# Performance work log

Measured on AMD Instinct MI355X. Metric: run time of the kernel, lower is better.

The kernel has to match this reference:

```python
import jax, jax.numpy as jnp
import numpy as np

N = 100_000      # n_nodes
DEG = 32         # edge_threshold (fixed out-degree)
D = 64           # in_channels = out_channels, heads = 1
NEG_SLOPE = 0.2


def setup_inputs() -> dict:
    key = jax.random.key(0)
    k1, k2, k3, k4 = jax.random.split(key, 4)
    x = jax.random.normal(k1, (N, D), jnp.float32)
    # fixed-degree edge list with no self loops (offset in [1, N-1])
    src = jnp.repeat(jnp.arange(N, dtype=jnp.int64), DEG)
    off = jax.random.randint(k2, (N * DEG,), 1, N, dtype=jnp.int64)
    dst = (src + off) % N
    edge_index = jnp.stack([src, dst])  # [2, E]
    # glorot init as in the torch module
    stdv_w = float(np.sqrt(6.0 / (D + D)))
    weight = jax.random.uniform(k3, (D, D), jnp.float32, -stdv_w, stdv_w)
    stdv_a = float(np.sqrt(6.0 / (1 + 2 * D)))  # att is [1, heads=1, 2*D]
    att = jax.random.uniform(k4, (2 * D,), jnp.float32, -stdv_a, stdv_a)
    bias = jnp.zeros((D,), jnp.float32)
    return {"x": x, "edge_index": edge_index, "weight": weight, "att": att, "bias": bias}


def reference(x, edge_index, weight, att, bias):
    n, d = x.shape
    h = x @ weight                               # [N, D] (heads=1)
    # add self loops (inputs are constructed without self loops)
    loop = jnp.arange(n, dtype=edge_index.dtype)
    src = jnp.concatenate([edge_index[0], loop])  # message sources (x_j)
    dst = jnp.concatenate([edge_index[1], loop])  # aggregation targets (x_i)
    # GAT edge score: (cat([x_i, x_j]) * att).sum(-1) = h_i@a_i + h_j@a_j
    a_i, a_j = att[:d], att[d:]
    s_i = h @ a_i                                 # [N]
    s_j = h @ a_j                                 # [N]
    alpha = s_i[dst] + s_j[src]                   # [E+N]
    alpha = jnp.where(alpha > 0, alpha, NEG_SLOPE * alpha)  # leaky_relu
    # segment softmax over destination nodes (numerically stable)
    amax = jax.ops.segment_max(alpha, dst, num_segments=n)
    e = jnp.exp(alpha - amax[dst])
    denom = jax.ops.segment_sum(e, dst, num_segments=n)
    w = e / (denom[dst] + 1e-16)                  # [E+N]
    # weighted scatter-add aggregation of source features
    out = jax.ops.segment_sum(h[src] * w[:, None], dst, num_segments=n)  # [N, D]
    out = out + bias                              # head-mean is identity (heads=1)
    # dropout(p=0.5) is identity in eval mode; F.normalize (L2, dim=1, eps=1e-12)
    norm = jnp.linalg.norm(out, axis=1, keepdims=True)
    return out / jnp.maximum(norm, 1e-12)
```

## Files before the change

kernel.cpp:

```cpp
#include <hip/hip_runtime.h>
#include <math.h>

#define NEG_SLOPE 0.2f
#define NBINS_MAX 392
#define CURSOR_PAD 16
#define NCHB 512
#define CHUNK_B 6256
#define CAPL 44
#define STRL 45
#define BIN_CAP 8704
#define CAPN 72
#define STRN 73

__device__ __forceinline__ unsigned pk_bf16x2(float a, float b) {
    unsigned ua = __float_as_uint(a);
    ua = (ua + 0x7FFFu + ((ua >> 16) & 1u)) >> 16;
    unsigned ub = __float_as_uint(b);
    ub = (ub + 0x7FFFu + ((ub >> 16) & 1u)) & 0xFFFF0000u;
    return ua | ub;
}

__global__ __launch_bounds__(512) void k_linbin(
        const float* __restrict__ x, const float* __restrict__ W,
        const float* __restrict__ att,
        uint2* __restrict__ h16, float* __restrict__ si, float* __restrict__ sj,
        const int* __restrict__ src, const int* __restrict__ dst, int E, int nbins,
        int* __restrict__ bin_cursor, unsigned* __restrict__ bin_edges, int n)
{
    __shared__ unsigned bins[NBINS_MAX * STRL];
    __shared__ int cnt[NBINS_MAX];
    __shared__ int gbase[NBINS_MAX];

    int tid = threadIdx.x;

    if (blockIdx.x < NCHB) {
        int base = blockIdx.x * CHUNK_B;
        int cntE = E - base;
        if (cntE > CHUNK_B) cntE = CHUNK_B;
        if (cntE < 0) cntE = 0;
        int c4 = cntE >> 2;

        for (int b = tid; b < nbins; b += 512) cnt[b] = 0;
        __syncthreads();

#define PLACE(dd, ss) { int bb = (dd) >> 8; int c = atomicAdd(&cnt[bb], 1); \
        if (c < CAPL) bins[bb * STRL + c] = ((unsigned)((dd) & 255) << 17) | (unsigned)(ss); }
        {
            const int4* dst4 = (const int4*)(dst + base);
            const int4* src4 = (const int4*)(src + base);
            for (int i = tid; i < c4; i += 512) {
                int4 d4 = dst4[i];
                int4 s4 = src4[i];
                PLACE(d4.x, s4.x) PLACE(d4.y, s4.y) PLACE(d4.z, s4.z) PLACE(d4.w, s4.w)
            }
            for (int i = (c4 << 2) + tid; i < cntE; i += 512) {
                int dd = dst[base + i]; int ss = src[base + i];
                PLACE(dd, ss)
            }
        }
#undef PLACE
        __syncthreads();

        {
            int start = (blockIdx.x * 97) % nbins;
            for (int k = tid; k < nbins; k += 512) {
                int b = k + start;
                if (b >= nbins) b -= nbins;
                int c = cnt[b];
                if (c > CAPL) c = CAPL;
                int g = (c > 0) ? atomicAdd(&bin_cursor[b * CURSOR_PAD], c) : 0;
                int allow = BIN_CAP - g;
                if (allow < 0) allow = 0;
                if (c > allow) c = allow;
                cnt[b] = c;
                gbase[b] = b * BIN_CAP + g;
            }
        }
        __syncthreads();

        int lane = tid & 63;
        int wv = tid >> 6;
        for (int b = wv; b < nbins; b += 8) {
            int c = cnt[b];
            if (lane < c) bin_edges[gbase[b] + lane] = bins[b * STRL + lane];
        }
    } else {
        int lb = blockIdx.x - NCHB;
        int lane = tid & 63;
        int wv = tid >> 6;
        int q = lane >> 4;
        int f = lane & 15;

        const float4* W4 = (const float4*)W;
        float4 Wr[16];
#pragma unroll
        for (int kb = 0; kb < 16; ++kb)
            Wr[kb] = W4[(16 * q + kb) * 16 + f];

        const float4* att4 = (const float4*)att;
        float4 ai4 = att4[f];
        float4 aj4 = att4[16 + f];
        const float4* x4 = (const float4*)x;

        int row0 = (lb * 8 + wv) * 8;
        for (int r = 0; r < 8; ++r) {
            int row = row0 + r;
            if (row >= n) break;
            size_t xb = (size_t)row * 16 + 4 * q;
            float4 xq0 = x4[xb + 0];
            float4 xq1 = x4[xb + 1];
            float4 xq2 = x4[xb + 2];
            float4 xq3 = x4[xb + 3];
            float4 acc = {0.f, 0.f, 0.f, 0.f};
#define LSTEP(xc, kb) { float4 w4 = Wr[kb]; \
        acc.x = fmaf((xc), w4.x, acc.x); acc.y = fmaf((xc), w4.y, acc.y); \
        acc.z = fmaf((xc), w4.z, acc.z); acc.w = fmaf((xc), w4.w, acc.w); }
            LSTEP(xq0.x, 0)  LSTEP(xq0.y, 1)  LSTEP(xq0.z, 2)  LSTEP(xq0.w, 3)
            LSTEP(xq1.x, 4)  LSTEP(xq1.y, 5)  LSTEP(xq1.z, 6)  LSTEP(xq1.w, 7)
            LSTEP(xq2.x, 8)  LSTEP(xq2.y, 9)  LSTEP(xq2.z, 10) LSTEP(xq2.w, 11)
            LSTEP(xq3.x, 12) LSTEP(xq3.y, 13) LSTEP(xq3.z, 14) LSTEP(xq3.w, 15)
#undef LSTEP
            acc.x += __shfl_xor(acc.x, 16); acc.x += __shfl_xor(acc.x, 32);
            acc.y += __shfl_xor(acc.y, 16); acc.y += __shfl_xor(acc.y, 32);
            acc.z += __shfl_xor(acc.z, 16); acc.z += __shfl_xor(acc.z, 32);
            acc.w += __shfl_xor(acc.w, 16); acc.w += __shfl_xor(acc.w, 32);

            if (q == 0) {
                uint2 p;
                p.x = pk_bf16x2(acc.x, acc.y);
                p.y = pk_bf16x2(acc.z, acc.w);
                h16[(size_t)row * 16 + f] = p;
            }

            float p = acc.x * ai4.x + acc.y * ai4.y + acc.z * ai4.z + acc.w * ai4.w;
            float pq = acc.x * aj4.x + acc.y * aj4.y + acc.z * aj4.z + acc.w * aj4.w;
#pragma unroll
            for (int o = 8; o >= 1; o >>= 1) {
                p += __shfl_xor(p, o);
                pq += __shfl_xor(pq, o);
            }
            if (lane == 0) { si[row] = p; sj[row] = pq; }
        }
    }
}

__global__ __launch_bounds__(512) void k_csr(const int* __restrict__ bin_cursor,
        const unsigned* __restrict__ bin_edges, unsigned* __restrict__ cols,
        int* __restrict__ row_start, int* __restrict__ deg, int n)
{
    __shared__ unsigned slots[256 * STRN];
    __shared__ int cntv[256];
    __shared__ int offv[256];
    __shared__ int wsum[4];
    int b = blockIdx.x;
    int tid = threadIdx.x;
    int base = b * BIN_CAP;
    int cntE = bin_cursor[b * CURSOR_PAD];
    if (cntE > BIN_CAP) cntE = BIN_CAP;
    int c4 = cntE >> 2;

    if (tid < 256) cntv[tid] = 0;
    __syncthreads();

#define PUT(pkv) { unsigned pk = (pkv); int nl = (int)(pk >> 17); \
        int c = atomicAdd(&cntv[nl], 1); \
        if (c < CAPN) slots[nl * STRN + c] = pk & 0x1FFFFu; }
    {
        const uint4* be4 = (const uint4*)(bin_edges + base);
        for (int i = tid; i < c4; i += 512) {
            uint4 p = be4[i];
            PUT(p.x) PUT(p.y) PUT(p.z) PUT(p.w)
        }
        for (int i = (c4 << 2) + tid; i < cntE; i += 512)
            PUT(bin_edges[base + i])
    }
#undef PUT
    __syncthreads();

    int lane = tid & 63;
    int wv = tid >> 6;
    int s = 0, v = 0;
    if (tid < 256) {
        s = cntv[tid];
        if (s > CAPN) s = CAPN;
        v = s;
#pragma unroll
        for (int o = 1; o < 64; o <<= 1) {
            int t = __shfl_up(v, o);
            if (lane >= o) v += t;
        }
        if (lane == 63) wsum[wv] = v;
    }
    __syncthreads();
    if (tid < 256) {
        int woff = 0;
        for (int w = 0; w < wv; ++w) woff += wsum[w];
        int ex = v - s + woff;
        int gd = b * 256 + tid;
        if (gd < n) {
            row_start[gd] = base + ex;
            deg[gd] = s;
        }
        offv[tid] = ex;
        cntv[tid] = s;
    }
    __syncthreads();

    for (int nl = wv; nl < 256; nl += 8) {
        int c = cntv[nl];
        int ex = offv[nl];
        if (lane < c)      cols[base + ex + lane]      = slots[nl * STRN + lane];
        if (lane + 64 < c) cols[base + ex + lane + 64] = slots[nl * STRN + lane + 64];
    }
}

__global__ __launch_bounds__(256) void k_agg(const uint2* __restrict__ h16,
        const float* __restrict__ si, const float* __restrict__ sj,
        const int* __restrict__ row_start, const int* __restrict__ deg_arr,
        const unsigned* __restrict__ cols,
        const float* __restrict__ bias, float* __restrict__ out, int n)
{
    __shared__ int2 swArr[4][132];
    int lane = threadIdx.x & 63;
    int wv = threadIdx.x >> 6;
    int d = blockIdx.x * 4 + wv;
    if (d >= n) return;

    int dg = deg_arr[d];
    if (dg > 128) dg = 128;
    int rs = row_start[d];
    float sid = si[d];

    int s0 = 0, s1 = 0;
    float a0 = -1e30f, a1 = -1e30f;
    if (lane < dg) {
        s0 = (int)cols[rs + lane];
        float t = sid + sj[s0];
        a0 = t > 0.f ? t : NEG_SLOPE * t;
    }
    if (lane + 64 < dg) {
        s1 = (int)cols[rs + lane + 64];
        float t = sid + sj[s1];
        a1 = t > 0.f ? t : NEG_SLOPE * t;
    }
    float tself = sid + sj[d];
    float aself = tself > 0.f ? tself : NEG_SLOPE * tself;

    float m = fmaxf(fmaxf(a0, a1), aself);
#pragma unroll
    for (int o = 32; o >= 1; o >>= 1) m = fmaxf(m, __shfl_xor(m, o));

    float e0 = (lane < dg) ? __expf(a0 - m) : 0.f;
    float e1 = (lane + 64 < dg) ? __expf(a1 - m) : 0.f;
    float eself = __expf(aself - m);

    float dsum = e0 + e1;
#pragma unroll
    for (int o = 32; o >= 1; o >>= 1) dsum += __shfl_xor(dsum, o);
    dsum += eself;

    if (lane < dg) swArr[wv][lane] = make_int2(s0, __float_as_int(e0));
    if (lane + 64 < dg) swArr[wv][lane + 64] = make_int2(s1, __float_as_int(e1));
    if (lane == 0) swArr[wv][dg] = make_int2(d, __float_as_int(eself));
    int cntAll = dg + 1;

    int q = lane >> 4;
    int f = lane & 15;
    int fb = f << 3;
    const char* h8 = (const char*)h16;
    float4 acc0 = {0.f, 0.f, 0.f, 0.f};
    float4 acc1 = {0.f, 0.f, 0.f, 0.f};
    float4 acc2 = {0.f, 0.f, 0.f, 0.f};
    float4 acc3 = {0.f, 0.f, 0.f, 0.f};

#define GLOAD(e) (*(const uint2*)(h8 + (((unsigned)(e) << 7) | fb)))
#define UNPK_FMA(hv, wgt, acc) { \
        acc.x = fmaf((wgt), __uint_as_float((hv).x << 16), acc.x); \
        acc.y = fmaf((wgt), __uint_as_float((hv).x & 0xFFFF0000u), acc.y); \
        acc.z = fmaf((wgt), __uint_as_float((hv).y << 16), acc.z); \
        acc.w = fmaf((wgt), __uint_as_float((hv).y & 0xFFFF0000u), acc.w); }

    int j = q;
    for (; j + 12 < cntAll; j += 16) {
        int2 eA = swArr[wv][j];
        int2 eB = swArr[wv][j + 4];
        int2 eC = swArr[wv][j + 8];
        int2 eD = swArr[wv][j + 12];
        uint2 hA = GLOAD(eA.x);
        uint2 hB = GLOAD(eB.x);
        uint2 hC = GLOAD(eC.x);
        uint2 hD = GLOAD(eD.x);
        float wA = __int_as_float(eA.y);
        float wB = __int_as_float(eB.y);
        float wC = __int_as_float(eC.y);
        float wD = __int_as_float(eD.y);
        UNPK_FMA(hA, wA, acc0)
        UNPK_FMA(hB, wB, acc1)
        UNPK_FMA(hC, wC, acc2)
        UNPK_FMA(hD, wD, acc3)
    }
    for (; j + 4 < cntAll; j += 8) {
        int2 eA = swArr[wv][j];
        int2 eB = swArr[wv][j + 4];
        uint2 hA = GLOAD(eA.x);
        uint2 hB = GLOAD(eB.x);
        float wA = __int_as_float(eA.y);
        float wB = __int_as_float(eB.y);
        UNPK_FMA(hA, wA, acc0)
        UNPK_FMA(hB, wB, acc1)
    }
    if (j < cntAll) {
        int2 eA = swArr[wv][j];
        uint2 hA = GLOAD(eA.x);
        float wA = __int_as_float(eA.y);
        UNPK_FMA(hA, wA, acc0)
    }
#undef UNPK_FMA
#undef GLOAD

    acc0.x += acc1.x; acc0.y += acc1.y; acc0.z += acc1.z; acc0.w += acc1.w;
    acc2.x += acc3.x; acc2.y += acc3.y; acc2.z += acc3.z; acc2.w += acc3.w;
    acc0.x += acc2.x; acc0.y += acc2.y; acc0.z += acc2.z; acc0.w += acc2.w;

    acc0.x += __shfl_xor(acc0.x, 16); acc0.x += __shfl_xor(acc0.x, 32);
    acc0.y += __shfl_xor(acc0.y, 16); acc0.y += __shfl_xor(acc0.y, 32);
    acc0.z += __shfl_xor(acc0.z, 16); acc0.z += __shfl_xor(acc0.z, 32);
    acc0.w += __shfl_xor(acc0.w, 16); acc0.w += __shfl_xor(acc0.w, 32);

    float inv = 1.f / (dsum + 1e-16f);
    const float4* b4 = (const float4*)bias;
    float4 bb = b4[f];
    float4 o4;
    o4.x = acc0.x * inv + bb.x;
    o4.y = acc0.y * inv + bb.y;
    o4.z = acc0.z * inv + bb.z;
    o4.w = acc0.w * inv + bb.w;

    float nsq = o4.x * o4.x + o4.y * o4.y + o4.z * o4.z + o4.w * o4.w;
#pragma unroll
    for (int o = 8; o >= 1; o >>= 1) nsq += __shfl_xor(nsq, o);
    float rn = 1.f / fmaxf(sqrtf(nsq), 1e-12f);

    if (q == 0) {
        float4 res;
        res.x = o4.x * rn; res.y = o4.y * rn; res.z = o4.z * rn; res.w = o4.w * rn;
        ((float4*)out)[(size_t)d * 16 + f] = res;
    }
}

extern "C" void kernel_launch(void* const* d_in, const int* in_sizes, int n_in,
                              void* d_out, int out_size, void* d_ws, size_t ws_size,
                              hipStream_t stream)
{
    const float* x    = (const float*)d_in[0];
    const int*   ei   = (const int*)d_in[1];
    const float* W    = (const float*)d_in[2];
    const float* att  = (const float*)d_in[3];
    const float* bias = (const float*)d_in[4];
    float* out = (float*)d_out;

    int n = in_sizes[0] / 64;
    int E = in_sizes[1] / 2;
    const int* src = ei;
    const int* dst = ei + E;

    int nbins = (n + 255) >> 8;
    int NLIN = (n + 63) / 64;

    char* ws = (char*)d_ws;
#define CARVE(ptr, type, count) type* ptr = (type*)ws; \
        ws += (((size_t)(count) * sizeof(type)) + 255) & ~(size_t)255;
    CARVE(h16, uint2, (size_t)n * 16)
    CARVE(si, float, n)
    CARVE(sj, float, n)
    CARVE(row_start, int, n)
    CARVE(deg, int, n)
    CARVE(bin_cursor, int, (size_t)NBINS_MAX * CURSOR_PAD)
    CARVE(bin_edges, unsigned, (size_t)nbins * BIN_CAP)
    CARVE(cols, unsigned, (size_t)nbins * BIN_CAP)
#undef CARVE

    hipMemsetAsync(bin_cursor, 0, (size_t)NBINS_MAX * CURSOR_PAD * sizeof(int), stream);
    k_linbin<<<NCHB + NLIN, 512, 0, stream>>>(x, W, att, h16, si, sj,
                                              src, dst, E, nbins,
                                              bin_cursor, bin_edges, n);
    k_csr<<<nbins, 512, 0, stream>>>(bin_cursor, bin_edges, cols, row_start, deg, n);
    k_agg<<<(n + 3) / 4, 256, 0, stream>>>(h16, si, sj, row_start, deg, cols, bias, out, n);
}
```

Before: 224.2 us.

## Split binning by bin parity and fuse linear transform into CSR kernel

The edge binning pass now launches two blocks per chunk. Each block handles only the bins of one parity, which halves its shared-memory footprint and may allow more resident blocks. The node linear transform and score computation move out of the binning kernel and into the CSR-build kernel, so the dense GEMM work overlaps the CSR pass instead of the binning pass. The aggregation kernel also skips the second-half edge loads when degree is at most 64, and it uses two-wide float vector FMAs, possibly emitting packed FMA instructions. In exchange, every edge is read twice in binning, and the two workloads are rebalanced across launches.

```diff
diff --git a/kernel.cpp b/kernel.cpp
--- a/kernel.cpp
+++ b/kernel.cpp
@@ -3,14 +3,17 @@
 
 #define NEG_SLOPE 0.2f
 #define NBINS_MAX 392
+#define NBINS_H 196
 #define CURSOR_PAD 16
-#define NCHB 512
 #define CHUNK_B 6256
+#define NCHUNKS 512
 #define CAPL 44
 #define STRL 45
 #define BIN_CAP 8704
 #define CAPN 72
 #define STRN 73
+
+typedef float v2f __attribute__((ext_vector_type(2)));
 
 __device__ __forceinline__ unsigned pk_bf16x2(float a, float b) {
     unsigned ua = __float_as_uint(a);
@@ -20,74 +23,150 @@
     return ua | ub;
 }
 
-__global__ __launch_bounds__(512) void k_linbin(
+__global__ __launch_bounds__(512) void k_bin(const int* __restrict__ src,
+        const int* __restrict__ dst, int E, int nbins,
+        int* __restrict__ bin_cursor, unsigned* __restrict__ bin_edges)
+{
+    __shared__ unsigned bins[NBINS_H * STRL];
+    __shared__ int cnt[NBINS_H];
+    __shared__ int gbase[NBINS_H];
+
+    int tid = threadIdx.x;
+    int par = blockIdx.x & 1;
+    int chunk = blockIdx.x >> 1;
+    int base = chunk * CHUNK_B;
+    int cntE = E - base;
+    if (cntE > CHUNK_B) cntE = CHUNK_B;
+    if (cntE < 0) cntE = 0;
+    int c4 = cntE >> 2;
+
+    for (int b = tid; b < NBINS_H; b += 512) cnt[b] = 0;
+    __syncthreads();
+
+#define PLACE(dd, ss) { int bb = (dd) >> 8; if ((bb & 1) == par) { \
+        int hb = bb >> 1; int c = atomicAdd(&cnt[hb], 1); \
+        if (c < CAPL) bins[hb * STRL + c] = ((unsigned)((dd) & 255) << 17) | (unsigned)(ss); } }
+    {
+        const int4* dst4 = (const int4*)(dst + base);
+        const int4* src4 = (const int4*)(src + base);
+        for (int i = tid; i < c4; i += 512) {
+            int4 d4 = dst4[i];
+            int4 s4 = src4[i];
+            PLACE(d4.x, s4.x) PLACE(d4.y, s4.y) PLACE(d4.z, s4.z) PLACE(d4.w, s4.w)
+        }
+        for (int i = (c4 << 2) + tid; i < cntE; i += 512) {
+            int dd = dst[base + i]; int ss = src[base + i];
+            PLACE(dd, ss)
+        }
+    }
+#undef PLACE
+    __syncthreads();
+
+    {
+        int start = (blockIdx.x * 37) % NBINS_H;
+        for (int k = tid; k < NBINS_H; k += 512) {
+            int hb = k + start;
+            if (hb >= NBINS_H) hb -= NBINS_H;
+            int bb = 2 * hb + par;
+            if (bb >= nbins) { cnt[hb] = 0; continue; }
+            int c = cnt[hb];
+            if (c > CAPL) c = CAPL;
+            int g = (c > 0) ? atomicAdd(&bin_cursor[bb * CURSOR_PAD], c) : 0;
+            int allow = BIN_CAP - g;
+            if (allow < 0) allow = 0;
+            if (c > allow) c = allow;
+            cnt[hb] = c;
+            gbase[hb] = bb * BIN_CAP + g;
+        }
+    }
+    __syncthreads();
+
+    int lane = tid & 63;
+    int wv = tid >> 6;
+    for (int hb = wv; hb < NBINS_H; hb += 8) {
+        int c = cnt[hb];
+        if (lane < c) bin_edges[gbase[hb] + lane] = bins[hb * STRL + lane];
+    }
+}
+
+__global__ __launch_bounds__(512, 4) void k_csrlin(
+        const int* __restrict__ bin_cursor,
+        const unsigned* __restrict__ bin_edges, unsigned* __restrict__ cols,
+        int* __restrict__ row_start, int* __restrict__ deg,
         const float* __restrict__ x, const float* __restrict__ W,
         const float* __restrict__ att,
         uint2* __restrict__ h16, float* __restrict__ si, float* __restrict__ sj,
-        const int* __restrict__ src, const int* __restrict__ dst, int E, int nbins,
-        int* __restrict__ bin_cursor, unsigned* __restrict__ bin_edges, int n)
+        int nbins, int n)
 {
-    __shared__ unsigned bins[NBINS_MAX * STRL];
-    __shared__ int cnt[NBINS_MAX];
-    __shared__ int gbase[NBINS_MAX];
+    __shared__ unsigned slots[256 * STRN];
+    __shared__ int cntv[256];
+    __shared__ int offv[256];
+    __shared__ int wsum[4];
 
     int tid = threadIdx.x;
-
-    if (blockIdx.x < NCHB) {
-        int base = blockIdx.x * CHUNK_B;
-        int cntE = E - base;
-        if (cntE > CHUNK_B) cntE = CHUNK_B;
-        if (cntE < 0) cntE = 0;
+    int lane = tid & 63;
+    int wv = tid >> 6;
+
+    if (blockIdx.x < (unsigned)nbins) {
+        int b = blockIdx.x;
+        int base = b * BIN_CAP;
+        int cntE = bin_cursor[b * CURSOR_PAD];
+        if (cntE > BIN_CAP) cntE = BIN_CAP;
         int c4 = cntE >> 2;
 
-        for (int b = tid; b < nbins; b += 512) cnt[b] = 0;
+        if (tid < 256) cntv[tid] = 0;
         __syncthreads();
 
-#define PLACE(dd, ss) { int bb = (dd) >> 8; int c = atomicAdd(&cnt[bb], 1); \
-        if (c < CAPL) bins[bb * STRL + c] = ((unsigned)((dd) & 255) << 17) | (unsigned)(ss); }
+#define PUT(pkv) { unsigned pk = (pkv); int nl = (int)(pk >> 17); \
+        int c = atomicAdd(&cntv[nl], 1); \
+        if (c < CAPN) slots[nl * STRN + c] = pk & 0x1FFFFu; }
         {
-            const int4* dst4 = (const int4*)(dst + base);
-            const int4* src4 = (const int4*)(src + base);
+            const uint4* be4 = (const uint4*)(bin_edges + base);
             for (int i = tid; i < c4; i += 512) {
-                int4 d4 = dst4[i];
-                int4 s4 = src4[i];
-                PLACE(d4.x, s4.x) PLACE(d4.y, s4.y) PLACE(d4.z, s4.z) PLACE(d4.w, s4.w)
-            }
-            for (int i = (c4 << 2) + tid; i < cntE; i += 512) {
-                int dd = dst[base + i]; int ss = src[base + i];
-                PLACE(dd, ss)
-            }
-        }
-#undef PLACE
+                uint4 p = be4[i];
+                PUT(p.x) PUT(p.y) PUT(p.z) PUT(p.w)
+            }
+            for (int i = (c4 << 2) + tid; i < cntE; i += 512)
+                PUT(bin_edges[base + i])
+        }
+#undef PUT
         __syncthreads();
 
-        {
-            int start = (blockIdx.x * 97) % nbins;
-            for (int k = tid; k < nbins; k += 512) {
-                int b = k + start;
-                if (b >= nbins) b -= nbins;
-                int c = cnt[b];
-                if (c > CAPL) c = CAPL;
-                int g = (c > 0) ? atomicAdd(&bin_cursor[b * CURSOR_PAD], c) : 0;
-                int allow = BIN_CAP - g;
-                if (allow < 0) allow = 0;
-                if (c > allow) c = allow;
-                cnt[b] = c;
-                gbase[b] = b * BIN_CAP + g;
-            }
+        int s = 0, v = 0;
+        if (tid < 256) {
+            s = cntv[tid];
+            if (s > CAPN) s = CAPN;
+            v = s;
+#pragma unroll
+            for (int o = 1; o < 64; o <<= 1) {
+                int t = __shfl_up(v, o);
+                if (lane >= o) v += t;
+            }
+            if (lane == 63) wsum[wv] = v;
         }
         __syncthreads();
-
-        int lane = tid & 63;
-        int wv = tid >> 6;
-        for (int b = wv; b < nbins; b += 8) {
-            int c = cnt[b];
-            if (lane < c) bin_edges[gbase[b] + lane] = bins[b * STRL + lane];
+        if (tid < 256) {
+            int woff = 0;
+            for (int w = 0; w < wv; ++w) woff += wsum[w];
+            int ex = v - s + woff;
+            int gd = b * 256 + tid;
+            if (gd < n) {
+                row_start[gd] = base + ex;
+                deg[gd] = s;
+            }
+            offv[tid] = ex;
+            cntv[tid] = s;
+        }
+        __syncthreads();
+
+        for (int nl = wv; nl < 256; nl += 8) {
+            int c = cntv[nl];
+            int ex = offv[nl];
+            if (lane < c)      cols[base + ex + lane]      = slots[nl * STRN + lane];
+            if (lane + 64 < c) cols[base + ex + lane + 64] = slots[nl * STRN + lane + 64];
         }
     } else {
-        int lb = blockIdx.x - NCHB;
-        int lane = tid & 63;
-        int wv = tid >> 6;
+        int lb = blockIdx.x - nbins;
         int q = lane >> 4;
         int f = lane & 15;
 
@@ -144,76 +223,6 @@
     }
 }
 
-__global__ __launch_bounds__(512) void k_csr(const int* __restrict__ bin_cursor,
-        const unsigned* __restrict__ bin_edges, unsigned* __restrict__ cols,
-        int* __restrict__ row_start, int* __restrict__ deg, int n)
-{
-    __shared__ unsigned slots[256 * STRN];
-    __shared__ int cntv[256];
-    __shared__ int offv[256];
-    __shared__ int wsum[4];
-    int b = blockIdx.x;
-    int tid = threadIdx.x;
-    int base = b * BIN_CAP;
-    int cntE = bin_cursor[b * CURSOR_PAD];
-    if (cntE > BIN_CAP) cntE = BIN_CAP;
-    int c4 = cntE >> 2;
-
-    if (tid < 256) cntv[tid] = 0;
-    __syncthreads();
-
-#define PUT(pkv) { unsigned pk = (pkv); int nl = (int)(pk >> 17); \
-        int c = atomicAdd(&cntv[nl], 1); \
-        if (c < CAPN) slots[nl * STRN + c] = pk & 0x1FFFFu; }
-    {
-        const uint4* be4 = (const uint4*)(bin_edges + base);
-        for (int i = tid; i < c4; i += 512) {
-            uint4 p = be4[i];
-            PUT(p.x) PUT(p.y) PUT(p.z) PUT(p.w)
-        }
-        for (int i = (c4 << 2) + tid; i < cntE; i += 512)
-            PUT(bin_edges[base + i])
-    }
-#undef PUT
-    __syncthreads();
-
-    int lane = tid & 63;
-    int wv = tid >> 6;
-    int s = 0, v = 0;
-    if (tid < 256) {
-        s = cntv[tid];
-        if (s > CAPN) s = CAPN;
-        v = s;
-#pragma unroll
-        for (int o = 1; o < 64; o <<= 1) {
-            int t = __shfl_up(v, o);
-            if (lane >= o) v += t;
-        }
-        if (lane == 63) wsum[wv] = v;
-    }
-    __syncthreads();
-    if (tid < 256) {
-        int woff = 0;
-        for (int w = 0; w < wv; ++w) woff += wsum[w];
-        int ex = v - s + woff;
-        int gd = b * 256 + tid;
-        if (gd < n) {
-            row_start[gd] = base + ex;
-            deg[gd] = s;
-        }
-        offv[tid] = ex;
-        cntv[tid] = s;
-    }
-    __syncthreads();
-
-    for (int nl = wv; nl < 256; nl += 8) {
-        int c = cntv[nl];
-        int ex = offv[nl];
-        if (lane < c)      cols[base + ex + lane]      = slots[nl * STRN + lane];
-        if (lane + 64 < c) cols[base + ex + lane + 64] = slots[nl * STRN + lane + 64];
-    }
-}
-
 __global__ __launch_bounds__(256) void k_agg(const uint2* __restrict__ h16,
         const float* __restrict__ si, const float* __restrict__ sj,
         const int* __restrict__ row_start, const int* __restrict__ deg_arr,
@@ -230,18 +239,21 @@
     if (dg > 128) dg = 128;
     int rs = row_start[d];
     float sid = si[d];
+    bool hi = dg > 64;
 
     int s0 = 0, s1 = 0;
-    float a0 = -1e30f, a1 = -1e30f;
+    float a0 = -1e30f, a1 = -1e30f, e1 = 0.f;
     if (lane < dg) {
         s0 = (int)cols[rs + lane];
         float t = sid + sj[s0];
         a0 = t > 0.f ? t : NEG_SLOPE * t;
     }
-    if (lane + 64 < dg) {
-        s1 = (int)cols[rs + lane + 64];
-        float t = sid + sj[s1];
-        a1 = t > 0.f ? t : NEG_SLOPE * t;
+    if (hi) {
+        if (lane + 64 < dg) {
+            s1 = (int)cols[rs + lane + 64];
+            float t = sid + sj[s1];
+            a1 = t > 0.f ? t : NEG_SLOPE * t;
+        }
     }
     float tself = sid + sj[d];
     float aself = tself > 0.f ? tself : NEG_SLOPE * tself;
@@ -251,7 +263,7 @@
     for (int o = 32; o >= 1; o >>= 1) m = fmaxf(m, __shfl_xor(m, o));
 
     float e0 = (lane < dg) ? __expf(a0 - m) : 0.f;
-    float e1 = (lane + 64 < dg) ? __expf(a1 - m) : 0.f;
+    if (hi) e1 = (lane + 64 < dg) ? __expf(a1 - m) : 0.f;
     float eself = __expf(aself - m);
 
     float dsum = e0 + e1;
@@ -260,7 +272,7 @@
     dsum += eself;
 
     if (lane < dg) swArr[wv][lane] = make_int2(s0, __float_as_int(e0));
-    if (lane + 64 < dg) swArr[wv][lane + 64] = make_int2(s1, __float_as_int(e1));
+    if (hi) { if (lane + 64 < dg) swArr[wv][lane + 64] = make_int2(s1, __float_as_int(e1)); }
     if (lane == 0) swArr[wv][dg] = make_int2(d, __float_as_int(eself));
     int cntAll = dg + 1;
 
@@ -268,17 +280,19 @@
     int f = lane & 15;
     int fb = f << 3;
     const char* h8 = (const char*)h16;
-    float4 acc0 = {0.f, 0.f, 0.f, 0.f};
-    float4 acc1 = {0.f, 0.f, 0.f, 0.f};
-    float4 acc2 = {0.f, 0.f, 0.f, 0.f};
-    float4 acc3 = {0.f, 0.f, 0.f, 0.f};
+    v2f aA0 = {0.f, 0.f}, aB0 = {0.f, 0.f};
+    v2f aA1 = {0.f, 0.f}, aB1 = {0.f, 0.f};
+    v2f aA2 = {0.f, 0.f}, aB2 = {0.f, 0.f};
+    v2f aA3 = {0.f, 0.f}, aB3 = {0.f, 0.f};
 
 #define GLOAD(e) (*(const uint2*)(h8 + (((unsigned)(e) << 7) | fb)))
-#define UNPK_FMA(hv, wgt, acc) { \
-        acc.x = fmaf((wgt), __uint_as_float((hv).x << 16), acc.x); \
-        acc.y = fmaf((wgt), __uint_as_float((hv).x & 0xFFFF0000u), acc.y); \
-        acc.z = fmaf((wgt), __uint_as_float((hv).y << 16), acc.z); \
-        acc.w = fmaf((wgt), __uint_as_float((hv).y & 0xFFFF0000u), acc.w); }
+#define UNPK_FMA(hv, wgt, accA, accB) { \
+        v2f h01, h23, w2; \
+        h01.x = __uint_as_float((hv).x << 16); h01.y = __uint_as_float((hv).x & 0xFFFF0000u); \
+        h23.x = __uint_as_float((hv).y << 16); h23.y = __uint_as_float((hv).y & 0xFFFF0000u); \
+        w2.x = (wgt); w2.y = (wgt); \
+        accA = w2 * h01 + accA; \
+        accB = w2 * h23 + accB; }
 
     int j = q;
     for (; j + 12 < cntAll; j += 16) {
@@ -290,37 +304,33 @@
         uint2 hB = GLOAD(eB.x);
         uint2 hC = GLOAD(eC.x);
         uint2 hD = GLOAD(eD.x);
-        float wA = __int_as_float(eA.y);
-        float wB = __int_as_float(eB.y);
-        float wC = __int_as_float(eC.y);
-        float wD = __int_as_float(eD.y);
-        UNPK_FMA(hA, wA, acc0)
-        UNPK_FMA(hB, wB, acc1)
-        UNPK_FMA(hC, wC, acc2)
-        UNPK_FMA(hD, wD, acc3)
+        UNPK_FMA(hA, __int_as_float(eA.y), aA0, aB0)
+        UNPK_FMA(hB, __int_as_float(eB.y), aA1, aB1)
+        UNPK_FMA(hC, __int_as_float(eC.y), aA2, aB2)
+        UNPK_FMA(hD, __int_as_float(eD.y), aA3, aB3)
     }
     for (; j + 4 < cntAll; j += 8) {
         int2 eA = swArr[wv][j];
         int2 eB = swArr[wv][j + 4];
         uint2 hA = GLOAD(eA.x);
         uint2 hB = GLOAD(eB.x);
-        float wA = __int_as_float(eA.y);
-        float wB = __int_as_float(eB.y);
-        UNPK_FMA(hA, wA, acc0)
-        UNPK_FMA(hB, wB, acc1)
+        UNPK_FMA(hA, __int_as_float(eA.y), aA0, aB0)
+        UNPK_FMA(hB, __int_as_float(eB.y), aA1, aB1)
     }
     if (j < cntAll) {
         int2 eA = swArr[wv][j];
         uint2 hA = GLOAD(eA.x);
-        float wA = __int_as_float(eA.y);
-        UNPK_FMA(hA, wA, acc0)
+        UNPK_FMA(hA, __int_as_float(eA.y), aA0, aB0)
     }
 #undef UNPK_FMA
 #undef GLOAD
 
-    acc0.x += acc1.x; acc0.y += acc1.y; acc0.z += acc1.z; acc0.w += acc1.w;
-    acc2.x += acc3.x; acc2.y += acc3.y; acc2.z += acc3.z; acc2.w += acc3.w;
-    acc0.x += acc2.x; acc0.y += acc2.y; acc0.z += acc2.z; acc0.w += acc2.w;
+    aA0 += aA1; aB0 += aB1;
+    aA2 += aA3; aB2 += aB3;
+    aA0 += aA2; aB0 += aB2;
+
+    float4 acc0;
+    acc0.x = aA0.x; acc0.y = aA0.y; acc0.z = aB0.x; acc0.w = aB0.y;
 
     acc0.x += __shfl_xor(acc0.x, 16); acc0.x += __shfl_xor(acc0.x, 32);
     acc0.y += __shfl_xor(acc0.y, 16); acc0.y += __shfl_xor(acc0.y, 32);
@@ -381,9 +391,9 @@
 #undef CARVE
 
     hipMemsetAsync(bin_cursor, 0, (size_t)NBINS_MAX * CURSOR_PAD * sizeof(int), stream);
-    k_linbin<<<NCHB + NLIN, 512, 0, stream>>>(x, W, att, h16, si, sj,
-                                              src, dst, E, nbins,
-                                              bin_cursor, bin_edges, n);
-    k_csr<<<nbins, 512, 0, stream>>>(bin_cursor, bin_edges, cols, row_start, deg, n);
+    k_bin<<<2 * NCHUNKS, 512, 0, stream>>>(src, dst, E, nbins, bin_cursor, bin_edges);
+    k_csrlin<<<nbins + NLIN, 512, 0, stream>>>(bin_cursor, bin_edges, cols,
+                                               row_start, deg,
+                                               x, W, att, h16, si, sj, nbins, n);
     k_agg<<<(n + 3) / 4, 256, 0, stream>>>(h16, si, sj, row_start, deg, cols, bias, out, n);
 }
```

After: 225.3 us. No clear change (+0.5%).
